# Kernel optimization log

Hardware: AMD Instinct MI355X
Metric: run time of the kernel (lower is better)

The kernel has to match this reference:

```python
import jax, jax.numpy as jnp
import numpy as np

B, LQ, LK, D = 32, 2048, 2048, 64


def setup_inputs() -> dict:
    key = jax.random.key(0)
    k1, k2, k3, k4 = jax.random.split(key, 4)
    querys = jax.random.normal(k1, (B, LQ, D), dtype=jnp.float32)
    keys = jax.random.normal(k2, (B, LK, D), dtype=jnp.float32)
    values = jax.random.normal(k3, (B, LK, D), dtype=jnp.float32)
    # valid lengths in [1, LK]
    valid_lens = jax.random.randint(k4, (B,), 1, LK + 1, dtype=jnp.int32)
    return {"querys": querys, "keys": keys, "values": values, "valid_lens": valid_lens}


def reference(querys, keys, values, valid_lens):
    d = querys.shape[-1]
    # [B, Lq, Lk] score matrix
    scores = jnp.einsum("bqd,bkd->bqk", querys, keys) / jnp.sqrt(jnp.asarray(d, querys.dtype))
    # masked softmax: key positions >= valid_len get -1e6 (as in d2l masked_softmax)
    key_pos = jnp.arange(scores.shape[-1], dtype=jnp.int32)  # [Lk]
    mask = key_pos[None, None, :] < valid_lens[:, None, None]  # [B, 1, Lk]
    scores = jnp.where(mask, scores, jnp.asarray(-1e6, scores.dtype))
    attn = jax.nn.softmax(scores, axis=-1)
    # dropout p=0.0 -> identity
    return jnp.einsum("bqk,bkd->bqd", attn, values)
```

## Files before the change

### kernel.cpp

```cpp
#include <hip/hip_runtime.h>
#include <hip/hip_bf16.h>
#include <math.h>


#define B_    32
#define LQ_   2048
#define LK_   2048
#define D_    64
#define SLOTF (64 * 64 + 64)
#define MBIAS 16.0f

typedef __attribute__((ext_vector_type(8)))  short bf16x8;
typedef __attribute__((ext_vector_type(4)))  float f32x4;
typedef __attribute__((ext_vector_type(16))) float f32x16;

#if defined(__has_builtin) && __has_builtin(__builtin_amdgcn_exp2f)
#define EXP2(x) __builtin_amdgcn_exp2f(x)
#else
#define EXP2(x) exp2f(x)
#endif

static __device__ __forceinline__ unsigned pk_bf16(float a, float b) {
    __hip_bfloat162 h = __float22bfloat162_rn(float2{a, b});
    return *(unsigned*)&h;
}

__global__ __launch_bounds__(128, 2) void fa_stage1(
    const float* __restrict__ Q, const float* __restrict__ K,
    const float* __restrict__ V, const int* __restrict__ vlen,
    float* __restrict__ O, float* __restrict__ ws,
    int nchunks, int chunk_len)
{
    __shared__ __align__(16) short Kl[64 * 64];
    __shared__ __align__(16) short Vt[64 * 64];

    const int tid  = threadIdx.x;
    const int wave = tid >> 6;
    const int lane = tid & 63;
    const int c31  = lane & 31;
    const int h    = lane >> 5;

    const int qt = blockIdx.x, b = blockIdx.y, cidx = blockIdx.z;
    const int vl = vlen[b];
    const int k_begin = cidx * chunk_len;
    if (k_begin >= vl) return;
    const int k_end = min(k_begin + chunk_len, vl);
    const int nt = (k_end - k_begin + 63) >> 6;
    const int q0 = qt * 64 + wave * 32;
    const int direct = (vl <= chunk_len);

    const float qscale = 0.125f * 1.44269504088896340736f;

    unsigned qfrag[4][4];
#pragma unroll
    for (int ks = 0; ks < 4; ++ks) {
        const float* qp = Q + ((size_t)(b * LQ_ + q0 + c31)) * D_ + ks * 16 + h * 8;
        f32x4 t0 = *(const f32x4*)qp;
        f32x4 t1 = *(const f32x4*)(qp + 4);
#pragma unroll
        for (int jj = 0; jj < 2; ++jj) {
            qfrag[ks][jj]     = pk_bf16(t0[2*jj] * qscale, t0[2*jj+1] * qscale);
            qfrag[ks][jj + 2] = pk_bf16(t1[2*jj] * qscale, t1[2*jj+1] * qscale);
        }
    }

    f32x16 oacc[2];
#pragma unroll
    for (int dt = 0; dt < 2; ++dt)
#pragma unroll
        for (int r = 0; r < 16; ++r) oacc[dt][r] = 0.f;
    float lrun = 0.f;

    const int skey = tid >> 1, skh = tid & 1;
    const int vkg  = tid & 7,  vdg = tid >> 3;

    const float* kgp = K + ((size_t)(b * LK_ + k_begin + skey)) * D_ + skh * 32;
    const float* vgp = V + ((size_t)(b * LK_ + k_begin + vkg * 8)) * D_ + vdg * 4;

    f32x4 kr[8], vr[8];
#pragma unroll
    for (int i = 0; i < 8; ++i) kr[i] = *(const f32x4*)(kgp + 4 * i);
#pragma unroll
    for (int i = 0; i < 8; ++i) vr[i] = *(const f32x4*)(vgp + (size_t)i * D_);

    for (int t = 0; t < nt; ++t) {
        const int k0 = k_begin + t * 64;
        if (t) __syncthreads();

        {
            unsigned pk32[16];
#pragma unroll
            for (int m = 0; m < 16; ++m)
                pk32[m] = pk_bf16(kr[m >> 1][2 * (m & 1)], kr[m >> 1][2 * (m & 1) + 1]);
#pragma unroll
            for (int cch = 0; cch < 4; ++cch) {
                const int pos = (skh * 4 + cch) ^ (skey & 7);
                *(bf16x8*)&Kl[skey * 64 + pos * 8] = *(bf16x8*)&pk32[4 * cch];
            }
#pragma unroll
            for (int dr = 0; dr < 4; ++dr) {
                unsigned w[4];
#pragma unroll
                for (int p = 0; p < 4; ++p)
                    w[p] = pk_bf16(vr[2 * p][dr], vr[2 * p + 1][dr]);
                const int dim = vdg * 4 + dr;
                const int pos = vkg ^ (dim & 7);
                *(bf16x8*)&Vt[dim * 64 + pos * 8] = *(bf16x8*)&w[0];
            }
        }
        if (t + 1 < nt) {
            const float* kn = kgp + (size_t)(t + 1) * 64 * D_;
            const float* vn = vgp + (size_t)(t + 1) * 64 * D_;
#pragma unroll
            for (int i = 0; i < 8; ++i) kr[i] = *(const f32x4*)(kn + 4 * i);
#pragma unroll
            for (int i = 0; i < 8; ++i) vr[i] = *(const f32x4*)(vn + (size_t)i * D_);
        }
        __syncthreads();

        f32x16 st[2];
#pragma unroll
        for (int s = 0; s < 2; ++s) {
#pragma unroll
            for (int r = 0; r < 16; ++r) st[s][r] = -MBIAS;
#pragma unroll
            for (int ks = 0; ks < 4; ++ks) {
                const int pos = (ks * 2 + h) ^ (c31 & 7);
                bf16x8 kf = *(const bf16x8*)&Kl[(s * 32 + c31) * 64 + pos * 8];
                st[s] = __builtin_amdgcn_mfma_f32_32x32x16_bf16(
                    kf, *(const bf16x8*)&qfrag[ks][0], st[s], 0, 0, 0);
            }
        }

        if (k0 + 64 > vl) {
#pragma unroll
            for (int s = 0; s < 2; ++s) {
                const int base = k0 + s * 32 + 4 * h;
#pragma unroll
                for (int r = 0; r < 16; ++r) {
                    const int key = base + (r & 3) + 8 * (r >> 2);
                    if (key >= vl) st[s][r] = -1e30f;
                }
            }
        }

        float rs0 = 0.f, rs1 = 0.f, rs2 = 0.f, rs3 = 0.f;
#pragma unroll
        for (int s = 0; s < 2; ++s)
#pragma unroll
            for (int g = 0; g < 4; ++g) {
                float p0 = EXP2(st[s][4*g]);
                float p1 = EXP2(st[s][4*g+1]);
                float p2 = EXP2(st[s][4*g+2]);
                float p3 = EXP2(st[s][4*g+3]);
                st[s][4*g] = p0; st[s][4*g+1] = p1; st[s][4*g+2] = p2; st[s][4*g+3] = p3;
                rs0 += p0; rs1 += p1; rs2 += p2; rs3 += p3;
            }
        float rs = (rs0 + rs1) + (rs2 + rs3);
        rs += __shfl_xor(rs, 32);
        lrun += rs;

        unsigned pk[2][8];
#pragma unroll
        for (int s = 0; s < 2; ++s)
#pragma unroll
            for (int m = 0; m < 8; ++m)
                pk[s][m] = pk_bf16(st[s][2 * m], st[s][2 * m + 1]);

#pragma unroll
        for (int kq = 0; kq < 4; ++kq) {
            const int s = kq >> 1, A4 = (kq & 1) * 4;
            unsigned p0 = pk[s][A4], p1 = pk[s][A4+1], p2 = pk[s][A4+2], p3 = pk[s][A4+3];
            unsigned xp0 = __shfl_xor((int)p0, 32);
            unsigned xp1 = __shfl_xor((int)p1, 32);
            unsigned xp2 = __shfl_xor((int)p2, 32);
            unsigned xp3 = __shfl_xor((int)p3, 32);
            unsigned pf[4];
            pf[0] = h ? xp2 : p0;
            pf[1] = h ? xp3 : p1;
            pf[2] = h ? p2  : xp0;
            pf[3] = h ? p3  : xp1;
            const bf16x8 pfr = *(const bf16x8*)&pf[0];
#pragma unroll
            for (int dt = 0; dt < 2; ++dt) {
                const int pos = (kq * 2 + h) ^ (c31 & 7);
                bf16x8 vf = *(const bf16x8*)&Vt[(dt * 32 + c31) * 64 + pos * 8];
                oacc[dt] = __builtin_amdgcn_mfma_f32_32x32x16_bf16(vf, pfr, oacc[dt], 0, 0, 0);
            }
        }
    }

    if (direct) {
        const float inv = 1.f / lrun;
        float* op = O + ((size_t)(b * LQ_ + q0 + c31)) * D_;
#pragma unroll
        for (int dt = 0; dt < 2; ++dt)
#pragma unroll
            for (int g = 0; g < 4; ++g) {
                f32x4 v;
#pragma unroll
                for (int j = 0; j < 4; ++j) v[j] = oacc[dt][4 * g + j] * inv;
                *(f32x4*)(op + dt * 32 + 8 * g + 4 * h) = v;
            }
    } else {
        float* base = ws + (size_t)((b * 32 + qt) * nchunks + cidx) * SLOTF;
        float* pp = base + (size_t)(wave * 32 + c31) * D_;
#pragma unroll
        for (int dt = 0; dt < 2; ++dt)
#pragma unroll
            for (int g = 0; g < 4; ++g) {
                f32x4 v;
#pragma unroll
                for (int j = 0; j < 4; ++j) v[j] = oacc[dt][4 * g + j];
                *(f32x4*)(pp + dt * 32 + 8 * g + 4 * h) = v;
            }
        if (h == 0)
            base[64 * 64 + wave * 32 + c31] = lrun;
    }
}

__global__ __launch_bounds__(256) void fa_combine(
    const float* __restrict__ ws, const int* __restrict__ vlen,
    float* __restrict__ O, int nchunks, int chunk_len)
{
    const int idx = blockIdx.x * 256 + threadIdx.x;
    const int b  = idx >> 15;
    const int vl = vlen[b];
    if (vl <= chunk_len) return;
    const int r  = idx & 32767;
    const int q  = r >> 4;
    const int dg = r & 15;
    const int nc = min(nchunks, (vl + chunk_len - 1) / chunk_len);
    const int qt = q >> 6, ql = q & 63;
    const size_t sbase = (size_t)((b * 32 + qt) * nchunks) * SLOTF;

    f32x4 acc = (f32x4){0.f, 0.f, 0.f, 0.f};
    float L = 0.f;
    for (int c = 0; c < nc; ++c) {
        const float* sb = ws + sbase + (size_t)c * SLOTF;
        L += sb[64 * 64 + ql];
        f32x4 o4 = *(const f32x4*)(sb + (size_t)ql * D_ + dg * 4);
        acc += o4;
    }
    const float inv = 1.f / L;
    *(f32x4*)(O + (size_t)(b * LQ_ + q) * D_ + dg * 4) = acc * inv;
}

extern "C" void kernel_launch(void* const* d_in, const int* in_sizes, int n_in,
                              void* d_out, int out_size, void* d_ws, size_t ws_size,
                              hipStream_t stream) {
    const float* Q    = (const float*)d_in[0];
    const float* K    = (const float*)d_in[1];
    const float* V    = (const float*)d_in[2];
    const int*   vlen = (const int*)d_in[3];
    float*       O    = (float*)d_out;
    float*       ws   = (float*)d_ws;

    int S = 4;
    while (S > 1 && (size_t)B_ * 32 * S * SLOTF * 4 > ws_size) S >>= 1;
    const int chunk_len = LK_ / S;

    dim3 grid(LQ_ / 64, B_, S);
    fa_stage1<<<grid, dim3(128), 0, stream>>>(Q, K, V, vlen, O, ws, S, chunk_len);
    if (S > 1) {
        const int nthreads = B_ * LQ_ * 16;
        fa_combine<<<dim3(nthreads / 256), dim3(256), 0, stream>>>(ws, vlen, O, S, chunk_len);
    }
}
```

Baseline: 176.0 us.

## Load K/V fragments directly from global memory, dropping LDS staging and barriers

Removes the shared-memory staging of K and V tiles. Each wave now loads its MFMA operand fragments directly from global fp32 memory and converts them to bf16 in registers, which eliminates both __syncthreads per tile. The block grows to 4 waves covering 128 queries, and the workspace is re-indexed per 32-query wave. The trade-off is that every wave reloads the same K/V data from global or L2 with no intra-block sharing. The V loads are strided scalar reads, which adds memory traffic and latency that is no longer software-prefetched.

```diff
diff --git a/kernel.cpp b/kernel.cpp
--- a/kernel.cpp
+++ b/kernel.cpp
@@ -7,7 +7,7 @@
 #define LQ_   2048
 #define LK_   2048
 #define D_    64
-#define SLOTF (64 * 64 + 64)
+#define SLOTW (32 * 64 + 32)
 #define MBIAS 16.0f
 
 typedef __attribute__((ext_vector_type(8)))  short bf16x8;
@@ -25,28 +25,26 @@
     return *(unsigned*)&h;
 }
 
-__global__ __launch_bounds__(128, 2) void fa_stage1(
+__global__ __launch_bounds__(256, 2) void fa_stage1(
     const float* __restrict__ Q, const float* __restrict__ K,
     const float* __restrict__ V, const int* __restrict__ vlen,
     float* __restrict__ O, float* __restrict__ ws,
     int nchunks, int chunk_len)
 {
-    __shared__ __align__(16) short Kl[64 * 64];
-    __shared__ __align__(16) short Vt[64 * 64];
-
     const int tid  = threadIdx.x;
     const int wave = tid >> 6;
     const int lane = tid & 63;
     const int c31  = lane & 31;
     const int h    = lane >> 5;
 
-    const int qt = blockIdx.x, b = blockIdx.y, cidx = blockIdx.z;
+    const int b = blockIdx.y, cidx = blockIdx.z;
     const int vl = vlen[b];
     const int k_begin = cidx * chunk_len;
     if (k_begin >= vl) return;
     const int k_end = min(k_begin + chunk_len, vl);
     const int nt = (k_end - k_begin + 63) >> 6;
-    const int q0 = qt * 64 + wave * 32;
+    const int q0 = blockIdx.x * 128 + wave * 32;
+    const int qw = q0 >> 5;
     const int direct = (vl <= chunk_len);
 
     const float qscale = 0.125f * 1.44269504088896340736f;
@@ -71,64 +69,24 @@
         for (int r = 0; r < 16; ++r) oacc[dt][r] = 0.f;
     float lrun = 0.f;
 
-    const int skey = tid >> 1, skh = tid & 1;
-    const int vkg  = tid & 7,  vdg = tid >> 3;
-
-    const float* kgp = K + ((size_t)(b * LK_ + k_begin + skey)) * D_ + skh * 32;
-    const float* vgp = V + ((size_t)(b * LK_ + k_begin + vkg * 8)) * D_ + vdg * 4;
-
-    f32x4 kr[8], vr[8];
-#pragma unroll
-    for (int i = 0; i < 8; ++i) kr[i] = *(const f32x4*)(kgp + 4 * i);
-#pragma unroll
-    for (int i = 0; i < 8; ++i) vr[i] = *(const f32x4*)(vgp + (size_t)i * D_);
-
     for (int t = 0; t < nt; ++t) {
         const int k0 = k_begin + t * 64;
-        if (t) __syncthreads();
-
-        {
-            unsigned pk32[16];
-#pragma unroll
-            for (int m = 0; m < 16; ++m)
-                pk32[m] = pk_bf16(kr[m >> 1][2 * (m & 1)], kr[m >> 1][2 * (m & 1) + 1]);
-#pragma unroll
-            for (int cch = 0; cch < 4; ++cch) {
-                const int pos = (skh * 4 + cch) ^ (skey & 7);
-                *(bf16x8*)&Kl[skey * 64 + pos * 8] = *(bf16x8*)&pk32[4 * cch];
-            }
-#pragma unroll
-            for (int dr = 0; dr < 4; ++dr) {
-                unsigned w[4];
-#pragma unroll
-                for (int p = 0; p < 4; ++p)
-                    w[p] = pk_bf16(vr[2 * p][dr], vr[2 * p + 1][dr]);
-                const int dim = vdg * 4 + dr;
-                const int pos = vkg ^ (dim & 7);
-                *(bf16x8*)&Vt[dim * 64 + pos * 8] = *(bf16x8*)&w[0];
-            }
-        }
-        if (t + 1 < nt) {
-            const float* kn = kgp + (size_t)(t + 1) * 64 * D_;
-            const float* vn = vgp + (size_t)(t + 1) * 64 * D_;
-#pragma unroll
-            for (int i = 0; i < 8; ++i) kr[i] = *(const f32x4*)(kn + 4 * i);
-#pragma unroll
-            for (int i = 0; i < 8; ++i) vr[i] = *(const f32x4*)(vn + (size_t)i * D_);
-        }
-        __syncthreads();
 
         f32x16 st[2];
+        const float* krow = K + ((size_t)(b * LK_ + k0 + c31)) * D_ + h * 8;
 #pragma unroll
         for (int s = 0; s < 2; ++s) {
 #pragma unroll
             for (int r = 0; r < 16; ++r) st[s][r] = -MBIAS;
+            const float* kp = krow + (size_t)s * 32 * D_;
 #pragma unroll
             for (int ks = 0; ks < 4; ++ks) {
-                const int pos = (ks * 2 + h) ^ (c31 & 7);
-                bf16x8 kf = *(const bf16x8*)&Kl[(s * 32 + c31) * 64 + pos * 8];
+                f32x4 a0 = *(const f32x4*)(kp + ks * 16);
+                f32x4 a1 = *(const f32x4*)(kp + ks * 16 + 4);
+                unsigned kw[4] = { pk_bf16(a0[0], a0[1]), pk_bf16(a0[2], a0[3]),
+                                   pk_bf16(a1[0], a1[1]), pk_bf16(a1[2], a1[3]) };
                 st[s] = __builtin_amdgcn_mfma_f32_32x32x16_bf16(
-                    kf, *(const bf16x8*)&qfrag[ks][0], st[s], 0, 0, 0);
+                    *(const bf16x8*)kw, *(const bf16x8*)&qfrag[ks][0], st[s], 0, 0, 0);
             }
         }
 
@@ -169,6 +127,20 @@
 
 #pragma unroll
         for (int kq = 0; kq < 4; ++kq) {
+            const float* vp = V + ((size_t)(b * LK_ + k0 + kq * 16 + h * 8)) * D_ + c31;
+            float v0[8], v1[8];
+#pragma unroll
+            for (int j = 0; j < 8; ++j) {
+                v0[j] = vp[(size_t)j * D_];
+                v1[j] = vp[(size_t)j * D_ + 32];
+            }
+            unsigned vw0[4], vw1[4];
+#pragma unroll
+            for (int jj = 0; jj < 4; ++jj) {
+                vw0[jj] = pk_bf16(v0[2*jj], v0[2*jj+1]);
+                vw1[jj] = pk_bf16(v1[2*jj], v1[2*jj+1]);
+            }
+
             const int s = kq >> 1, A4 = (kq & 1) * 4;
             unsigned p0 = pk[s][A4], p1 = pk[s][A4+1], p2 = pk[s][A4+2], p3 = pk[s][A4+3];
             unsigned xp0 = __shfl_xor((int)p0, 32);
@@ -181,12 +153,11 @@
             pf[2] = h ? p2  : xp0;
             pf[3] = h ? p3  : xp1;
             const bf16x8 pfr = *(const bf16x8*)&pf[0];
-#pragma unroll
-            for (int dt = 0; dt < 2; ++dt) {
-                const int pos = (kq * 2 + h) ^ (c31 & 7);
-                bf16x8 vf = *(const bf16x8*)&Vt[(dt * 32 + c31) * 64 + pos * 8];
-                oacc[dt] = __builtin_amdgcn_mfma_f32_32x32x16_bf16(vf, pfr, oacc[dt], 0, 0, 0);
-            }
+
+            oacc[0] = __builtin_amdgcn_mfma_f32_32x32x16_bf16(
+                *(const bf16x8*)vw0, pfr, oacc[0], 0, 0, 0);
+            oacc[1] = __builtin_amdgcn_mfma_f32_32x32x16_bf16(
+                *(const bf16x8*)vw1, pfr, oacc[1], 0, 0, 0);
         }
     }
 
@@ -203,8 +174,8 @@
                 *(f32x4*)(op + dt * 32 + 8 * g + 4 * h) = v;
             }
     } else {
-        float* base = ws + (size_t)((b * 32 + qt) * nchunks + cidx) * SLOTF;
-        float* pp = base + (size_t)(wave * 32 + c31) * D_;
+        float* base = ws + (size_t)((b * 64 + qw) * nchunks + cidx) * SLOTW;
+        float* pp = base + (size_t)c31 * D_;
 #pragma unroll
         for (int dt = 0; dt < 2; ++dt)
 #pragma unroll
@@ -215,7 +186,7 @@
                 *(f32x4*)(pp + dt * 32 + 8 * g + 4 * h) = v;
             }
         if (h == 0)
-            base[64 * 64 + wave * 32 + c31] = lrun;
+            base[32 * 64 + c31] = lrun;
     }
 }
 
@@ -231,14 +202,14 @@
     const int q  = r >> 4;
     const int dg = r & 15;
     const int nc = min(nchunks, (vl + chunk_len - 1) / chunk_len);
-    const int qt = q >> 6, ql = q & 63;
-    const size_t sbase = (size_t)((b * 32 + qt) * nchunks) * SLOTF;
+    const int qw = q >> 5, ql = q & 31;
+    const size_t sbase = (size_t)((b * 64 + qw) * nchunks) * SLOTW;
 
     f32x4 acc = (f32x4){0.f, 0.f, 0.f, 0.f};
     float L = 0.f;
     for (int c = 0; c < nc; ++c) {
-        const float* sb = ws + sbase + (size_t)c * SLOTF;
-        L += sb[64 * 64 + ql];
+        const float* sb = ws + sbase + (size_t)c * SLOTW;
+        L += sb[32 * 64 + ql];
         f32x4 o4 = *(const f32x4*)(sb + (size_t)ql * D_ + dg * 4);
         acc += o4;
     }
@@ -257,11 +228,11 @@
     float*       ws   = (float*)d_ws;
 
     int S = 4;
-    while (S > 1 && (size_t)B_ * 32 * S * SLOTF * 4 > ws_size) S >>= 1;
+    while (S > 1 && (size_t)B_ * 64 * S * SLOTW * 4 > ws_size) S >>= 1;
     const int chunk_len = LK_ / S;
 
-    dim3 grid(LQ_ / 64, B_, S);
-    fa_stage1<<<grid, dim3(128), 0, stream>>>(Q, K, V, vlen, O, ws, S, chunk_len);
+    dim3 grid(LQ_ / 128, B_, S);
+    fa_stage1<<<grid, dim3(256), 0, stream>>>(Q, K, V, vlen, O, ws, S, chunk_len);
     if (S > 1) {
         const int nthreads = B_ * LQ_ * 16;
         fa_combine<<<dim3(nthreads / 256), dim3(256), 0, stream>>>(ws, vlen, O, S, chunk_len);
```

Result: slower. 214.0 us (+21.6%).
